# Kernel optimization log

Measured on AMD Instinct MI355X. Metric: run time of the kernel, lower is better.

Reference implementation:

```python
import jax, jax.numpy as jnp
import numpy as np

N_PER_DEG = 30000
MAX_DEG = 6
MIN_DEG = 0
N_ATOMS = N_PER_DEG * (MAX_DEG + 1)  # 210000, atoms sorted by degree
N_FEAT = 128
NB_FILTER = 128
NB_AFFINE = 2 * MAX_DEG + (1 - MIN_DEG)  # 13


def setup_inputs() -> dict:
    key = jax.random.key(0)
    ks = jax.random.split(key, 2 + MAX_DEG)
    atoms = jax.random.normal(ks[0], (N_ATOMS, N_FEAT), dtype=jnp.float32)
    # glorot-ish scale for the 13 affine weights
    W = jax.random.normal(ks[1], (NB_AFFINE, N_FEAT, NB_FILTER), dtype=jnp.float32) * (1.0 / np.sqrt(N_FEAT))
    b = jnp.zeros((NB_AFFINE, NB_FILTER), dtype=jnp.float32)
    # deg_slice[d] = (start, count) for degree d in 0..MAX_DEG; equal-size buckets
    deg_slice = jnp.asarray(
        np.stack([np.arange(MAX_DEG + 1) * N_PER_DEG,
                  np.full(MAX_DEG + 1, N_PER_DEG)], axis=1).astype(np.int32))
    inp = {"atoms": atoms, "W": W, "b": b, "deg_slice": deg_slice}
    for d in range(1, MAX_DEG + 1):
        inp[f"adj{d}"] = jax.random.randint(ks[1 + d], (N_PER_DEG, d), 0, N_ATOMS, dtype=jnp.int32)
    return inp


def reference(atoms, W, b, deg_slice, adj1, adj2, adj3, adj4, adj5, adj6):
    """Degree-bucketed graph convolution (deepchem GraphConv, linear activation).

    W ordering matches the original iterator: for deg=1..MAX_DEG the pair
    (rel=W[2*(deg-1)], self=W[2*(deg-1)+1]), then deg-0 self uses W[2*MAX_DEG].
    Output concat order: deg 0 bucket first, then deg 1..MAX_DEG.
    """
    adjs = [adj1, adj2, adj3, adj4, adj5, adj6]
    ds = np.asarray(deg_slice)  # structural constant: static slice bounds
    outs = [None] * (MAX_DEG + 1 - MIN_DEG)
    # deg 0: self-affine only
    s0, c0 = int(ds[0, 0]), int(ds[0, 1])
    outs[0] = atoms[s0:s0 + c0] @ W[2 * MAX_DEG] + b[2 * MAX_DEG]
    for deg in range(1, MAX_DEG + 1):
        s, c = int(ds[deg, 0]), int(ds[deg, 1])
        # gather neighbors of each degree-deg atom and sum: (c, deg, F) -> (c, F)
        rel = jnp.take(atoms, adjs[deg - 1], axis=0).sum(axis=1)
        out = (rel @ W[2 * (deg - 1)] + b[2 * (deg - 1)]
               + atoms[s:s + c] @ W[2 * (deg - 1) + 1] + b[2 * (deg - 1) + 1])
        outs[deg] = out
    return jnp.concatenate(outs, axis=0)  # (N_ATOMS, NB_FILTER)
```

## Files before the change

### kernel.cpp

```cpp
#include <hip/hip_runtime.h>
#include <hip/hip_bf16.h>

#define NPD 30000
#define NF  128
#define MAXDEG 6
#define LDK2 264

#define WT_BLOCKS   208
#define CVT8_BLOCKS 1641

typedef __attribute__((ext_vector_type(8))) short short8;
typedef __attribute__((ext_vector_type(4))) float floatx4;

__device__ __forceinline__ unsigned short f2bf(float f) {
    __hip_bfloat16 h = __float2bfloat16(f);
    return __builtin_bit_cast(unsigned short, h);
}
__device__ __forceinline__ float bf2f(unsigned short u) {
    unsigned v = ((unsigned)u) << 16; return __builtin_bit_cast(float, v);
}
__device__ __forceinline__ uint4 pack16B(float4 a, float4 b) {
    uint4 v;
    v.x = (unsigned)f2bf(a.x) | ((unsigned)f2bf(a.y) << 16);
    v.y = (unsigned)f2bf(a.z) | ((unsigned)f2bf(a.w) << 16);
    v.z = (unsigned)f2bf(b.x) | ((unsigned)f2bf(b.y) << 16);
    v.w = (unsigned)f2bf(b.z) | ((unsigned)f2bf(b.w) << 16);
    return v;
}
__device__ __forceinline__ uint4 pack16Bv(floatx4 a, floatx4 b) {
    uint4 v;
    v.x = (unsigned)f2bf(a.x) | ((unsigned)f2bf(a.y) << 16);
    v.y = (unsigned)f2bf(a.z) | ((unsigned)f2bf(a.w) << 16);
    v.z = (unsigned)f2bf(b.x) | ((unsigned)f2bf(b.y) << 16);
    v.w = (unsigned)f2bf(b.z) | ((unsigned)f2bf(b.w) << 16);
    return v;
}
__device__ __forceinline__ void addu4(float* s, uint4 h) {
    s[0] += bf2f((unsigned short)h.x); s[1] += bf2f((unsigned short)(h.x >> 16));
    s[2] += bf2f((unsigned short)h.y); s[3] += bf2f((unsigned short)(h.y >> 16));
    s[4] += bf2f((unsigned short)h.z); s[5] += bf2f((unsigned short)(h.z >> 16));
    s[6] += bf2f((unsigned short)h.w); s[7] += bf2f((unsigned short)(h.w >> 16));
}

__device__ __forceinline__ void lgkm_barrier() {
    asm volatile("s_waitcnt lgkmcnt(0)" ::: "memory");
    __builtin_amdgcn_s_barrier();
}

__global__ __launch_bounds__(256) void prep_kernel(
    const float* __restrict__ atoms, const float* __restrict__ W,
    unsigned short* __restrict__ atomsH, unsigned short* __restrict__ Wt)
{
    __shared__ unsigned short t[32][33];
    const int bx = blockIdx.x;
    if (bx < WT_BLOCKS) {
        const int a  = bx >> 4;
        const int k0 = ((bx >> 2) & 3) * 32, n0 = (bx & 3) * 32;
        const int tx = threadIdx.x & 31, ty = threadIdx.x >> 5;
        const float*    Wp  = W  + (size_t)a * NF * NF;
        unsigned short* Wtp = Wt + (size_t)a * NF * NF;
#pragma unroll
        for (int i = 0; i < 32; i += 8)
            t[ty + i][tx] = f2bf(Wp[(size_t)(k0 + ty + i) * NF + (n0 + tx)]);
        __syncthreads();
#pragma unroll
        for (int i = 0; i < 32; i += 8)
            Wtp[(size_t)(n0 + ty + i) * NF + (k0 + tx)] = t[tx][ty + i];
    } else {
        const size_t n8   = (size_t)NPD * (MAXDEG + 1) * NF / 8;
        const size_t base = (size_t)(bx - WT_BLOCKS) * 2048 + threadIdx.x;
#pragma unroll
        for (int it = 0; it < 8; ++it) {
            const size_t i = base + (size_t)it * 256;
            if (i < n8) {
                const floatx4* p = (const floatx4*)(atoms + i * 8);
                floatx4 a = __builtin_nontemporal_load(p);
                floatx4 b = __builtin_nontemporal_load(p + 1);
                ((uint4*)atomsH)[i] = pack16Bv(a, b);
            }
        }
    }
}

template <int DEG, bool BF16A>
__device__ __forceinline__ void fused_work(
    const float* __restrict__ atomsF, const unsigned short* __restrict__ atomsH,
    const unsigned short* __restrict__ Wt, const float* __restrict__ bvec,
    const int* __restrict__ adj, float* __restrict__ out,
    unsigned short* __restrict__ sA, int bx)
{
    const int tid  = threadIdx.x;
    const int lane = tid & 63, wave = tid >> 6;
    const int nb = lane & 15;
    const int kq = (lane >> 4) * 8;
    const int col0 = wave * 32;
    const int row0 = bx * 32;
    const int valid = min(32, NPD - row0);
    const int row0g = DEG * NPD + row0;
    const int wi_self = (DEG == 0) ? 12 : (2 * DEG - 1);
    const int wi_rel  = (DEG > 0) ? 2 * (DEG - 1) : 0;

    floatx4 acc[2][2];
#pragma unroll
    for (int i = 0; i < 2; i++)
#pragma unroll
        for (int j = 0; j < 2; j++) acc[i][j] = (floatx4){0.f, 0.f, 0.f, 0.f};

    const int r0 = tid >> 4,  ch0 = (tid & 15) * 8;
    const int r1 = r0 + 16;
    const int rr0 = min(r0, valid - 1), rr1 = min(r1, valid - 1);

    auto mma4_pre = [&](const short8 bs[4][2], int aoff) {
#pragma unroll
        for (int kk = 0; kk < 4; ++kk) {
            short8 af[2];
#pragma unroll
            for (int mt = 0; mt < 2; ++mt)
                af[mt] = *(const short8*)&sA[(mt * 16 + nb) * LDK2 + aoff + kk * 32 + kq];
#pragma unroll
            for (int mt = 0; mt < 2; ++mt)
#pragma unroll
                for (int nt = 0; nt < 2; ++nt)
                    acc[mt][nt] = __builtin_amdgcn_mfma_f32_16x16x32_bf16(
                        af[mt], bs[kk][nt], acc[mt][nt], 0, 0, 0);
        }
    };
    auto mma4_ld = [&](int wi, int aoff) {
        const unsigned short* Wp = Wt + (size_t)wi * NF * NF;
#pragma unroll
        for (int kk = 0; kk < 4; ++kk) {
            short8 bfr[2];
#pragma unroll
            for (int nt = 0; nt < 2; ++nt)
                bfr[nt] = *(const short8*)(Wp + (size_t)(col0 + nt * 16 + nb) * NF
                                              + kk * 32 + kq);
            short8 af[2];
#pragma unroll
            for (int mt = 0; mt < 2; ++mt)
                af[mt] = *(const short8*)&sA[(mt * 16 + nb) * LDK2 + aoff + kk * 32 + kq];
#pragma unroll
            for (int mt = 0; mt < 2; ++mt)
#pragma unroll
                for (int nt = 0; nt < 2; ++nt)
                    acc[mt][nt] = __builtin_amdgcn_mfma_f32_16x16x32_bf16(
                        af[mt], bfr[nt], acc[mt][nt], 0, 0, 0);
        }
    };

    if constexpr (BF16A) {
        uint4 s0 = *(const uint4*)(atomsH + (size_t)(row0g + rr0) * NF + ch0);
        uint4 s1 = *(const uint4*)(atomsH + (size_t)(row0g + rr1) * NF + ch0);

        const int gr  = tid >> 3;
        const int gc  = (tid & 7) * 16;
        const int grr = min(gr, valid - 1);

        int idxs[DEG > 0 ? DEG : 1];
        if constexpr (DEG > 0) {
            const int* arow = adj + (size_t)(row0 + grr) * DEG;
#pragma unroll
            for (int j = 0; j < DEG; ++j) idxs[j] = arow[j];
        }

        short8 bs[4][2];
        {
            const unsigned short* Wp = Wt + (size_t)wi_self * NF * NF;
#pragma unroll
            for (int kk = 0; kk < 4; ++kk)
#pragma unroll
                for (int nt = 0; nt < 2; ++nt)
                    bs[kk][nt] = *(const short8*)(Wp + (size_t)(col0 + nt * 16 + nb) * NF
                                                     + kk * 32 + kq);
        }

        if constexpr (DEG > 0) {
            uint4 ga[DEG], gb[DEG];
#pragma unroll
            for (int j = 0; j < DEG; ++j) {
                const unsigned short* base = atomsH + (size_t)idxs[j] * NF + gc;
                ga[j] = *(const uint4*)base;
                gb[j] = *(const uint4*)(base + 8);
            }

            *(uint4*)&sA[r0 * LDK2 + ch0] = s0;
            *(uint4*)&sA[r1 * LDK2 + ch0] = s1;
            lgkm_barrier();

            mma4_pre(bs, 0);

            float s[16];
#pragma unroll
            for (int i = 0; i < 16; ++i) s[i] = 0.f;
#pragma unroll
            for (int j = 0; j < DEG; ++j) { addu4(s, ga[j]); addu4(s + 8, gb[j]); }
            uint4 w0 = pack16B(make_float4(s[0], s[1], s[2], s[3]),
                               make_float4(s[4], s[5], s[6], s[7]));
            uint4 w1 = pack16B(make_float4(s[8], s[9], s[10], s[11]),
                               make_float4(s[12], s[13], s[14], s[15]));
            *(uint4*)&sA[gr * LDK2 + NF + gc]     = w0;
            *(uint4*)&sA[gr * LDK2 + NF + gc + 8] = w1;
            lgkm_barrier();

            mma4_ld(wi_rel, NF);
        } else {
            *(uint4*)&sA[r0 * LDK2 + ch0] = s0;
            *(uint4*)&sA[r1 * LDK2 + ch0] = s1;
            lgkm_barrier();
            mma4_pre(bs, 0);
        }
    } else {
        const float4* sp0 = (const float4*)(atomsF + (size_t)(row0g + rr0) * NF + ch0);
        const float4* sp1 = (const float4*)(atomsF + (size_t)(row0g + rr1) * NF + ch0);
        float4 a0 = sp0[0], a1 = sp0[1], a2 = sp1[0], a3 = sp1[1];
        *(uint4*)&sA[r0 * LDK2 + ch0] = pack16B(a0, a1);
        *(uint4*)&sA[r1 * LDK2 + ch0] = pack16B(a2, a3);
        if constexpr (DEG > 0) {
            const int gr  = tid >> 3;
            const int gc  = (tid & 7) * 16;
            const int grr = min(gr, valid - 1);
            const int* arow = adj + (size_t)(row0 + grr) * DEG;
            int idxs[DEG];
#pragma unroll
            for (int j = 0; j < DEG; ++j) idxs[j] = arow[j];
            float s[16];
#pragma unroll
            for (int i = 0; i < 16; ++i) s[i] = 0.f;
            float4 q0, q1, q2, q3, n0, n1, n2, n3;
            {
                const float4* p = (const float4*)(atomsF + (size_t)idxs[0] * NF + gc);
                q0 = p[0]; q1 = p[1]; q2 = p[2]; q3 = p[3];
            }
#pragma unroll
            for (int j = 0; j < DEG; ++j) {
                if (j + 1 < DEG) {
                    const float4* p = (const float4*)(atomsF + (size_t)idxs[j + 1] * NF + gc);
                    n0 = p[0]; n1 = p[1]; n2 = p[2]; n3 = p[3];
                }
                s[0]  += q0.x; s[1]  += q0.y; s[2]  += q0.z; s[3]  += q0.w;
                s[4]  += q1.x; s[5]  += q1.y; s[6]  += q1.z; s[7]  += q1.w;
                s[8]  += q2.x; s[9]  += q2.y; s[10] += q2.z; s[11] += q2.w;
                s[12] += q3.x; s[13] += q3.y; s[14] += q3.z; s[15] += q3.w;
                q0 = n0; q1 = n1; q2 = n2; q3 = n3;
            }
            uint4 w0 = pack16B(make_float4(s[0], s[1], s[2], s[3]),
                               make_float4(s[4], s[5], s[6], s[7]));
            uint4 w1 = pack16B(make_float4(s[8], s[9], s[10], s[11]),
                               make_float4(s[12], s[13], s[14], s[15]));
            *(uint4*)&sA[gr * LDK2 + NF + gc]     = w0;
            *(uint4*)&sA[gr * LDK2 + NF + gc + 8] = w1;
        }
        __syncthreads();
        mma4_ld(wi_self, 0);
        if constexpr (DEG > 0) mma4_ld(wi_rel, NF);
    }

    float bias[2];
#pragma unroll
    for (int nt = 0; nt < 2; ++nt) {
        const int n = col0 + nt * 16 + nb;
        float bv = bvec[wi_self * NF + n];
        if (DEG > 0) bv += bvec[wi_rel * NF + n];
        bias[nt] = bv;
    }
    const int rq = (lane >> 4) * 4;
#pragma unroll
    for (int mt = 0; mt < 2; ++mt) {
#pragma unroll
        for (int reg = 0; reg < 4; ++reg) {
            const int r = mt * 16 + rq + reg;
            if (r < valid) {
                float* op = out + (size_t)(row0g + r) * NF;
#pragma unroll
                for (int nt = 0; nt < 2; ++nt)
                    __builtin_nontemporal_store(acc[mt][nt][reg] + bias[nt],
                                                op + col0 + nt * 16 + nb);
            }
        }
    }
}

template <bool BF16A>
__global__ __launch_bounds__(256) void fused_kernel(
    const float* __restrict__ atomsF, const unsigned short* __restrict__ atomsH,
    const unsigned short* __restrict__ Wt, const float* __restrict__ bvec,
    const int* __restrict__ adj1, const int* __restrict__ adj2,
    const int* __restrict__ adj3, const int* __restrict__ adj4,
    const int* __restrict__ adj5, const int* __restrict__ adj6,
    float* __restrict__ out)
{
    __shared__ unsigned short sA[32 * LDK2];
    const int bid = blockIdx.x;
    const int deg = bid % 7, bx = bid / 7;
    switch (deg) {
        case 0: fused_work<0, BF16A>(atomsF, atomsH, Wt, bvec, nullptr, out, sA, bx); break;
        case 1: fused_work<1, BF16A>(atomsF, atomsH, Wt, bvec, adj1,    out, sA, bx); break;
        case 2: fused_work<2, BF16A>(atomsF, atomsH, Wt, bvec, adj2,    out, sA, bx); break;
        case 3: fused_work<3, BF16A>(atomsF, atomsH, Wt, bvec, adj3,    out, sA, bx); break;
        case 4: fused_work<4, BF16A>(atomsF, atomsH, Wt, bvec, adj4,    out, sA, bx); break;
        case 5: fused_work<5, BF16A>(atomsF, atomsH, Wt, bvec, adj5,    out, sA, bx); break;
        default: fused_work<6, BF16A>(atomsF, atomsH, Wt, bvec, adj6,   out, sA, bx); break;
    }
}

__global__ __launch_bounds__(128) void naive_kernel(
    const float* __restrict__ atoms, const float* __restrict__ W,
    const float* __restrict__ b,
    const int* __restrict__ adj1, const int* __restrict__ adj2,
    const int* __restrict__ adj3, const int* __restrict__ adj4,
    const int* __restrict__ adj5, const int* __restrict__ adj6,
    float* __restrict__ out)
{
    const int i = blockIdx.x;
    const int deg = i / NPD, r = i - deg * NPD, n = threadIdx.x;
    __shared__ float selfr[NF], relr[NF];
    selfr[n] = atoms[(size_t)i * NF + n];
    float rv = 0.f;
    if (deg > 0) {
        const int* adjs[6] = {adj1, adj2, adj3, adj4, adj5, adj6};
        const int* adj = adjs[deg - 1];
        for (int j = 0; j < deg; ++j)
            rv += atoms[(size_t)adj[(size_t)r * deg + j] * NF + n];
    }
    relr[n] = rv;
    __syncthreads();
    const int ws  = (deg == 0) ? 12 : 2 * deg - 1;
    const int wrl = 2 * (deg - 1);
    float acc = b[ws * NF + n] + ((deg > 0) ? b[wrl * NF + n] : 0.f);
    for (int k = 0; k < NF; ++k) {
        acc += selfr[k] * W[(size_t)ws * NF * NF + (size_t)k * NF + n];
        if (deg > 0) acc += relr[k] * W[(size_t)wrl * NF * NF + (size_t)k * NF + n];
    }
    out[(size_t)i * NF + n] = acc;
}

extern "C" void kernel_launch(void* const* d_in, const int* in_sizes, int n_in,
                              void* d_out, int out_size, void* d_ws, size_t ws_size,
                              hipStream_t stream) {
    const float* atoms = (const float*)d_in[0];
    const float* W     = (const float*)d_in[1];
    const float* b     = (const float*)d_in[2];
    const int* adj1 = (const int*)d_in[4];
    const int* adj2 = (const int*)d_in[5];
    const int* adj3 = (const int*)d_in[6];
    const int* adj4 = (const int*)d_in[7];
    const int* adj5 = (const int*)d_in[8];
    const int* adj6 = (const int*)d_in[9];

    const size_t wt_bytes = (size_t)13 * NF * NF * sizeof(unsigned short);
    const size_t at_bytes = (size_t)NPD * (MAXDEG + 1) * NF * sizeof(unsigned short);
    const int gx = (NPD + 31) / 32;

    if (ws_size >= wt_bytes + at_bytes) {
        unsigned short* Wt     = (unsigned short*)d_ws;
        unsigned short* atomsH = (unsigned short*)((char*)d_ws + wt_bytes);
        prep_kernel<<<WT_BLOCKS + CVT8_BLOCKS, 256, 0, stream>>>(atoms, W, atomsH, Wt);
        fused_kernel<true><<<gx * 7, 256, 0, stream>>>(
            atoms, atomsH, Wt, b, adj1, adj2, adj3, adj4, adj5, adj6, (float*)d_out);
    } else if (ws_size >= wt_bytes) {
        unsigned short* Wt = (unsigned short*)d_ws;
        prep_kernel<<<WT_BLOCKS, 256, 0, stream>>>(atoms, W, nullptr, Wt);
        fused_kernel<false><<<gx * 7, 256, 0, stream>>>(
            atoms, nullptr, Wt, b, adj1, adj2, adj3, adj4, adj5, adj6, (float*)d_out);
    } else {
        naive_kernel<<<NPD * (MAXDEG + 1), NF, 0, stream>>>(
            atoms, W, b, adj1, adj2, adj3, adj4, adj5, adj6, (float*)d_out);
    }
}
```

Measured before the change: 264.6 us.

## Process two 32-row tiles per block, reusing self weights and prefetching next tile

Each block now handles 64 rows as two sequential 32-row tiles, halving the grid. The self-weight fragments held in registers are reused for both tiles, and the second tile's self rows and adjacency indices are loaded while the first tile's MFMAs and epilogue run. The aim is to amortise per-block weight loads and launch overhead and to overlap gather latency with compute. The cost is higher register pressure and fewer blocks, which can reduce occupancy and latency hiding.

```diff
diff --git a/kernel.cpp b/kernel.cpp
--- a/kernel.cpp
+++ b/kernel.cpp
@@ -94,22 +94,24 @@
     const int nb = lane & 15;
     const int kq = (lane >> 4) * 8;
     const int col0 = wave * 32;
-    const int row0 = bx * 32;
-    const int valid = min(32, NPD - row0);
+    const int row0 = bx * 64;
+    const int v0 = min(32, NPD - row0);
+    const int v1 = min(32, NPD - row0 - 32);
     const int row0g = DEG * NPD + row0;
     const int wi_self = (DEG == 0) ? 12 : (2 * DEG - 1);
     const int wi_rel  = (DEG > 0) ? 2 * (DEG - 1) : 0;
 
-    floatx4 acc[2][2];
-#pragma unroll
-    for (int i = 0; i < 2; i++)
-#pragma unroll
-        for (int j = 0; j < 2; j++) acc[i][j] = (floatx4){0.f, 0.f, 0.f, 0.f};
-
     const int r0 = tid >> 4,  ch0 = (tid & 15) * 8;
     const int r1 = r0 + 16;
-    const int rr0 = min(r0, valid - 1), rr1 = min(r1, valid - 1);
-
+    const int gr = tid >> 3,  gc = (tid & 7) * 16;
+
+    floatx4 acc[2][2];
+    auto zacc = [&]() {
+#pragma unroll
+        for (int i = 0; i < 2; i++)
+#pragma unroll
+            for (int j = 0; j < 2; j++) acc[i][j] = (floatx4){0.f, 0.f, 0.f, 0.f};
+    };
     auto mma4_pre = [&](const short8 bs[4][2], int aoff) {
 #pragma unroll
         for (int kk = 0; kk < 4; ++kk) {
@@ -146,114 +148,6 @@
                         af[mt], bfr[nt], acc[mt][nt], 0, 0, 0);
         }
     };
-
-    if constexpr (BF16A) {
-        uint4 s0 = *(const uint4*)(atomsH + (size_t)(row0g + rr0) * NF + ch0);
-        uint4 s1 = *(const uint4*)(atomsH + (size_t)(row0g + rr1) * NF + ch0);
-
-        const int gr  = tid >> 3;
-        const int gc  = (tid & 7) * 16;
-        const int grr = min(gr, valid - 1);
-
-        int idxs[DEG > 0 ? DEG : 1];
-        if constexpr (DEG > 0) {
-            const int* arow = adj + (size_t)(row0 + grr) * DEG;
-#pragma unroll
-            for (int j = 0; j < DEG; ++j) idxs[j] = arow[j];
-        }
-
-        short8 bs[4][2];
-        {
-            const unsigned short* Wp = Wt + (size_t)wi_self * NF * NF;
-#pragma unroll
-            for (int kk = 0; kk < 4; ++kk)
-#pragma unroll
-                for (int nt = 0; nt < 2; ++nt)
-                    bs[kk][nt] = *(const short8*)(Wp + (size_t)(col0 + nt * 16 + nb) * NF
-                                                     + kk * 32 + kq);
-        }
-
-        if constexpr (DEG > 0) {
-            uint4 ga[DEG], gb[DEG];
-#pragma unroll
-            for (int j = 0; j < DEG; ++j) {
-                const unsigned short* base = atomsH + (size_t)idxs[j] * NF + gc;
-                ga[j] = *(const uint4*)base;
-                gb[j] = *(const uint4*)(base + 8);
-            }
-
-            *(uint4*)&sA[r0 * LDK2 + ch0] = s0;
-            *(uint4*)&sA[r1 * LDK2 + ch0] = s1;
-            lgkm_barrier();
-
-            mma4_pre(bs, 0);
-
-            float s[16];
-#pragma unroll
-            for (int i = 0; i < 16; ++i) s[i] = 0.f;
-#pragma unroll
-            for (int j = 0; j < DEG; ++j) { addu4(s, ga[j]); addu4(s + 8, gb[j]); }
-            uint4 w0 = pack16B(make_float4(s[0], s[1], s[2], s[3]),
-                               make_float4(s[4], s[5], s[6], s[7]));
-            uint4 w1 = pack16B(make_float4(s[8], s[9], s[10], s[11]),
-                               make_float4(s[12], s[13], s[14], s[15]));
-            *(uint4*)&sA[gr * LDK2 + NF + gc]     = w0;
-            *(uint4*)&sA[gr * LDK2 + NF + gc + 8] = w1;
-            lgkm_barrier();
-
-            mma4_ld(wi_rel, NF);
-        } else {
-            *(uint4*)&sA[r0 * LDK2 + ch0] = s0;
-            *(uint4*)&sA[r1 * LDK2 + ch0] = s1;
-            lgkm_barrier();
-            mma4_pre(bs, 0);
-        }
-    } else {
-        const float4* sp0 = (const float4*)(atomsF + (size_t)(row0g + rr0) * NF + ch0);
-        const float4* sp1 = (const float4*)(atomsF + (size_t)(row0g + rr1) * NF + ch0);
-        float4 a0 = sp0[0], a1 = sp0[1], a2 = sp1[0], a3 = sp1[1];
-        *(uint4*)&sA[r0 * LDK2 + ch0] = pack16B(a0, a1);
-        *(uint4*)&sA[r1 * LDK2 + ch0] = pack16B(a2, a3);
-        if constexpr (DEG > 0) {
-            const int gr  = tid >> 3;
-            const int gc  = (tid & 7) * 16;
-            const int grr = min(gr, valid - 1);
-            const int* arow = adj + (size_t)(row0 + grr) * DEG;
-            int idxs[DEG];
-#pragma unroll
-            for (int j = 0; j < DEG; ++j) idxs[j] = arow[j];
-            float s[16];
-#pragma unroll
-            for (int i = 0; i < 16; ++i) s[i] = 0.f;
-            float4 q0, q1, q2, q3, n0, n1, n2, n3;
-            {
-                const float4* p = (const float4*)(atomsF + (size_t)idxs[0] * NF + gc);
-                q0 = p[0]; q1 = p[1]; q2 = p[2]; q3 = p[3];
-            }
-#pragma unroll
-            for (int j = 0; j < DEG; ++j) {
-                if (j + 1 < DEG) {
-                    const float4* p = (const float4*)(atomsF + (size_t)idxs[j + 1] * NF + gc);
-                    n0 = p[0]; n1 = p[1]; n2 = p[2]; n3 = p[3];
-                }
-                s[0]  += q0.x; s[1]  += q0.y; s[2]  += q0.z; s[3]  += q0.w;
-                s[4]  += q1.x; s[5]  += q1.y; s[6]  += q1.z; s[7]  += q1.w;
-                s[8]  += q2.x; s[9]  += q2.y; s[10] += q2.z; s[11] += q2.w;
-                s[12] += q3.x; s[13] += q3.y; s[14] += q3.z; s[15] += q3.w;
-                q0 = n0; q1 = n1; q2 = n2; q3 = n3;
-            }
-            uint4 w0 = pack16B(make_float4(s[0], s[1], s[2], s[3]),
-                               make_float4(s[4], s[5], s[6], s[7]));
-            uint4 w1 = pack16B(make_float4(s[8], s[9], s[10], s[11]),
-                               make_float4(s[12], s[13], s[14], s[15]));
-            *(uint4*)&sA[gr * LDK2 + NF + gc]     = w0;
-            *(uint4*)&sA[gr * LDK2 + NF + gc + 8] = w1;
-        }
-        __syncthreads();
-        mma4_ld(wi_self, 0);
-        if constexpr (DEG > 0) mma4_ld(wi_rel, NF);
-    }
-
     float bias[2];
 #pragma unroll
     for (int nt = 0; nt < 2; ++nt) {
@@ -263,18 +157,171 @@
         bias[nt] = bv;
     }
     const int rq = (lane >> 4) * 4;
-#pragma unroll
-    for (int mt = 0; mt < 2; ++mt) {
-#pragma unroll
-        for (int reg = 0; reg < 4; ++reg) {
-            const int r = mt * 16 + rq + reg;
-            if (r < valid) {
-                float* op = out + (size_t)(row0g + r) * NF;
+    auto epilogue = [&](int vlim, int toff) {
+#pragma unroll
+        for (int mt = 0; mt < 2; ++mt) {
+#pragma unroll
+            for (int reg = 0; reg < 4; ++reg) {
+                const int r = mt * 16 + rq + reg;
+                if (r < vlim) {
+                    float* op = out + (size_t)(row0g + toff + r) * NF;
+#pragma unroll
+                    for (int nt = 0; nt < 2; ++nt)
+                        __builtin_nontemporal_store(acc[mt][nt][reg] + bias[nt],
+                                                    op + col0 + nt * 16 + nb);
+                }
+            }
+        }
+    };
+
+    if constexpr (BF16A) {
+        uint4 s0a = *(const uint4*)(atomsH + (size_t)(row0g + min(r0, v0 - 1)) * NF + ch0);
+        uint4 s0b = *(const uint4*)(atomsH + (size_t)(row0g + min(r1, v0 - 1)) * NF + ch0);
+
+        int idx0[DEG > 0 ? DEG : 1];
+        if constexpr (DEG > 0) {
+            const int* arow = adj + (size_t)(row0 + min(gr, v0 - 1)) * DEG;
+#pragma unroll
+            for (int j = 0; j < DEG; ++j) idx0[j] = arow[j];
+        }
+        short8 bs[4][2];
+        {
+            const unsigned short* Wp = Wt + (size_t)wi_self * NF * NF;
+#pragma unroll
+            for (int kk = 0; kk < 4; ++kk)
 #pragma unroll
                 for (int nt = 0; nt < 2; ++nt)
-                    __builtin_nontemporal_store(acc[mt][nt][reg] + bias[nt],
-                                                op + col0 + nt * 16 + nb);
-            }
+                    bs[kk][nt] = *(const short8*)(Wp + (size_t)(col0 + nt * 16 + nb) * NF
+                                                     + kk * 32 + kq);
+        }
+
+        if constexpr (DEG > 0) {
+            uint4 ga[DEG], gb[DEG];
+#pragma unroll
+            for (int j = 0; j < DEG; ++j) {
+                const unsigned short* base = atomsH + (size_t)idx0[j] * NF + gc;
+                ga[j] = *(const uint4*)base;
+                gb[j] = *(const uint4*)(base + 8);
+            }
+            *(uint4*)&sA[r0 * LDK2 + ch0] = s0a;
+            *(uint4*)&sA[r1 * LDK2 + ch0] = s0b;
+            lgkm_barrier();
+            zacc();
+            mma4_pre(bs, 0);
+
+            float s[16];
+#pragma unroll
+            for (int i = 0; i < 16; ++i) s[i] = 0.f;
+#pragma unroll
+            for (int j = 0; j < DEG; ++j) { addu4(s, ga[j]); addu4(s + 8, gb[j]); }
+            *(uint4*)&sA[gr * LDK2 + NF + gc]     = pack16B(
+                make_float4(s[0], s[1], s[2], s[3]), make_float4(s[4], s[5], s[6], s[7]));
+            *(uint4*)&sA[gr * LDK2 + NF + gc + 8] = pack16B(
+                make_float4(s[8], s[9], s[10], s[11]), make_float4(s[12], s[13], s[14], s[15]));
+
+            uint4 s1a, s1b;
+            int idx1[DEG];
+            if (v1 > 0) {
+                s1a = *(const uint4*)(atomsH + (size_t)(row0g + 32 + min(r0, v1 - 1)) * NF + ch0);
+                s1b = *(const uint4*)(atomsH + (size_t)(row0g + 32 + min(r1, v1 - 1)) * NF + ch0);
+                const int* arow1 = adj + (size_t)(row0 + 32 + min(gr, v1 - 1)) * DEG;
+#pragma unroll
+                for (int j = 0; j < DEG; ++j) idx1[j] = arow1[j];
+            }
+            lgkm_barrier();
+            mma4_ld(wi_rel, NF);
+            epilogue(v0, 0);
+
+            if (v1 > 0) {
+                uint4 ga1[DEG], gb1[DEG];
+#pragma unroll
+                for (int j = 0; j < DEG; ++j) {
+                    const unsigned short* base = atomsH + (size_t)idx1[j] * NF + gc;
+                    ga1[j] = *(const uint4*)base;
+                    gb1[j] = *(const uint4*)(base + 8);
+                }
+                lgkm_barrier();
+                *(uint4*)&sA[r0 * LDK2 + ch0] = s1a;
+                *(uint4*)&sA[r1 * LDK2 + ch0] = s1b;
+                lgkm_barrier();
+                zacc();
+                mma4_pre(bs, 0);
+
+                float s2[16];
+#pragma unroll
+                for (int i = 0; i < 16; ++i) s2[i] = 0.f;
+#pragma unroll
+                for (int j = 0; j < DEG; ++j) { addu4(s2, ga1[j]); addu4(s2 + 8, gb1[j]); }
+                *(uint4*)&sA[gr * LDK2 + NF + gc]     = pack16B(
+                    make_float4(s2[0], s2[1], s2[2], s2[3]),
+                    make_float4(s2[4], s2[5], s2[6], s2[7]));
+                *(uint4*)&sA[gr * LDK2 + NF + gc + 8] = pack16B(
+                    make_float4(s2[8], s2[9], s2[10], s2[11]),
+                    make_float4(s2[12], s2[13], s2[14], s2[15]));
+                lgkm_barrier();
+                mma4_ld(wi_rel, NF);
+                epilogue(v1, 32);
+            }
+        } else {
+            uint4 s1a, s1b;
+            if (v1 > 0) {
+                s1a = *(const uint4*)(atomsH + (size_t)(row0g + 32 + min(r0, v1 - 1)) * NF + ch0);
+                s1b = *(const uint4*)(atomsH + (size_t)(row0g + 32 + min(r1, v1 - 1)) * NF + ch0);
+            }
+            *(uint4*)&sA[r0 * LDK2 + ch0] = s0a;
+            *(uint4*)&sA[r1 * LDK2 + ch0] = s0b;
+            lgkm_barrier();
+            zacc();
+            mma4_pre(bs, 0);
+            epilogue(v0, 0);
+            if (v1 > 0) {
+                lgkm_barrier();
+                *(uint4*)&sA[r0 * LDK2 + ch0] = s1a;
+                *(uint4*)&sA[r1 * LDK2 + ch0] = s1b;
+                lgkm_barrier();
+                zacc();
+                mma4_pre(bs, 0);
+                epilogue(v1, 32);
+            }
+        }
+    } else {
+        for (int t = 0; t < 2; ++t) {
+            const int vt = (t == 0) ? v0 : v1;
+            if (vt <= 0) break;
+            const int toff = t * 32;
+            if (t) __syncthreads();
+            const float4* sp0 = (const float4*)(atomsF + (size_t)(row0g + toff + min(r0, vt - 1)) * NF + ch0);
+            const float4* sp1 = (const float4*)(atomsF + (size_t)(row0g + toff + min(r1, vt - 1)) * NF + ch0);
+            float4 a0 = sp0[0], a1 = sp0[1], a2 = sp1[0], a3 = sp1[1];
+            *(uint4*)&sA[r0 * LDK2 + ch0] = pack16B(a0, a1);
+            *(uint4*)&sA[r1 * LDK2 + ch0] = pack16B(a2, a3);
+            if constexpr (DEG > 0) {
+                const int* arow = adj + (size_t)(row0 + toff + min(gr, vt - 1)) * DEG;
+                int idxs[DEG];
+#pragma unroll
+                for (int j = 0; j < DEG; ++j) idxs[j] = arow[j];
+                float s[16];
+#pragma unroll
+                for (int i = 0; i < 16; ++i) s[i] = 0.f;
+#pragma unroll
+                for (int j = 0; j < DEG; ++j) {
+                    const float4* p = (const float4*)(atomsF + (size_t)idxs[j] * NF + gc);
+                    float4 q0 = p[0], q1 = p[1], q2 = p[2], q3 = p[3];
+                    s[0]  += q0.x; s[1]  += q0.y; s[2]  += q0.z; s[3]  += q0.w;
+                    s[4]  += q1.x; s[5]  += q1.y; s[6]  += q1.z; s[7]  += q1.w;
+                    s[8]  += q2.x; s[9]  += q2.y; s[10] += q2.z; s[11] += q2.w;
+                    s[12] += q3.x; s[13] += q3.y; s[14] += q3.z; s[15] += q3.w;
+                }
+                *(uint4*)&sA[gr * LDK2 + NF + gc]     = pack16B(
+                    make_float4(s[0], s[1], s[2], s[3]), make_float4(s[4], s[5], s[6], s[7]));
+                *(uint4*)&sA[gr * LDK2 + NF + gc + 8] = pack16B(
+                    make_float4(s[8], s[9], s[10], s[11]), make_float4(s[12], s[13], s[14], s[15]));
+            }
+            __syncthreads();
+            zacc();
+            mma4_ld(wi_self, 0);
+            if constexpr (DEG > 0) mma4_ld(wi_rel, NF);
+            epilogue(vt, toff);
         }
     }
 }
@@ -348,18 +395,18 @@
 
     const size_t wt_bytes = (size_t)13 * NF * NF * sizeof(unsigned short);
     const size_t at_bytes = (size_t)NPD * (MAXDEG + 1) * NF * sizeof(unsigned short);
-    const int gx = (NPD + 31) / 32;
+    const int gxB = (NPD + 63) / 64;
 
     if (ws_size >= wt_bytes + at_bytes) {
         unsigned short* Wt     = (unsigned short*)d_ws;
         unsigned short* atomsH = (unsigned short*)((char*)d_ws + wt_bytes);
         prep_kernel<<<WT_BLOCKS + CVT8_BLOCKS, 256, 0, stream>>>(atoms, W, atomsH, Wt);
-        fused_kernel<true><<<gx * 7, 256, 0, stream>>>(
+        fused_kernel<true><<<gxB * 7, 256, 0, stream>>>(
             atoms, atomsH, Wt, b, adj1, adj2, adj3, adj4, adj5, adj6, (float*)d_out);
     } else if (ws_size >= wt_bytes) {
         unsigned short* Wt = (unsigned short*)d_ws;
         prep_kernel<<<WT_BLOCKS, 256, 0, stream>>>(atoms, W, nullptr, Wt);
-        fused_kernel<false><<<gx * 7, 256, 0, stream>>>(
+        fused_kernel<false><<<gxB * 7, 256, 0, stream>>>(
             atoms, nullptr, Wt, b, adj1, adj2, adj3, adj4, adj5, adj6, (float*)d_out);
     } else {
         naive_kernel<<<NPD * (MAXDEG + 1), NF, 0, stream>>>(
```

New measurement: 258.9 us. -2.2%, faster.
